# Performance work log

Measured on AMD Instinct MI355X. Metric: run time of the kernel, lower is better.

The kernel has to match this reference:

```python
import jax, jax.numpy as jnp
import numpy as np

B, IN_DIM, D, H, L = 16, 4096, 100, 200, 4
N, E = B * IN_DIM, 8 * B * IN_DIM
EPS = 1e-7  # GENConv message eps


def setup_inputs() -> dict:
    key = jax.random.key(0)
    ks = jax.random.split(key, 16)
    s = 0.05
    return {
        "x": jax.random.normal(ks[0], (N, 1), jnp.float32),
        "edge_index": jax.random.randint(ks[1], (2, E), 0, N),
        "batch_ids": jnp.repeat(jnp.arange(B), IN_DIM),  # graphs of exactly IN_DIM nodes
        "enc_w": jax.random.normal(ks[2], (1, D), jnp.float32) * s,
        "enc_b": jnp.zeros((D,), jnp.float32),
        "h1_w": jax.random.normal(ks[3], (IN_DIM, 1000), jnp.float32) * 0.02,
        "h1_b": jnp.zeros((1000,), jnp.float32),
        "h2_w": jax.random.normal(ks[4], (1000, 100), jnp.float32) * s,
        "h2_b": jnp.zeros((100,), jnp.float32),
        "ln_g": jnp.ones((L, D), jnp.float32),
        "ln_b": jnp.zeros((L, D), jnp.float32),
        "w1": jax.random.normal(ks[5], (L, D, H), jnp.float32) * s,
        "b1": jnp.zeros((L, H), jnp.float32),
        "bn_g": jnp.ones((L, H), jnp.float32),
        "bn_b": jnp.zeros((L, H), jnp.float32),
        "w2": jax.random.normal(ks[6], (L, H, D), jnp.float32) * s,
        "b2": jnp.zeros((L, D), jnp.float32),
        "dec_w": jax.random.normal(ks[7], (D, 1), jnp.float32) * s,
        "dec_b": jnp.zeros((1,), jnp.float32),
    }


def reference(x, edge_index, batch_ids, enc_w, enc_b, h1_w, h1_b, h2_w, h2_b,
              ln_g, ln_b, w1, b1, bn_g, bn_b, w2, b2, dec_w, dec_b):
    src, dst = edge_index[0], edge_index[1]
    # dense branch: [B, IN_DIM] -> 1000 -> 100 with leaky_relu (dropout p=0)
    xs = x.reshape(B, IN_DIM)
    xs = jax.nn.leaky_relu(xs @ h1_w + h1_b, 0.01)
    xs = jax.nn.leaky_relu(xs @ h2_w + h2_b, 0.01)

    h = x @ enc_w + enc_b  # node encoder -> [N, D]
    for i in range(L):  # DeepGCNLayer res+: x + GENConv(dropout(relu(LN(x))))
        mu = jnp.mean(h, axis=-1, keepdims=True)
        var = jnp.mean((h - mu) ** 2, axis=-1, keepdims=True)
        hn = (h - mu) * jax.lax.rsqrt(var + 1e-5) * ln_g[i] + ln_b[i]
        hn = jnp.maximum(hn, 0.0)  # act (dropout in eval mode = identity)
        # GENConv: message = relu(x_j) + eps, softmax aggregation (t=1)
        m = jnp.maximum(hn[src], 0.0) + EPS            # [E, D]
        mx = jax.ops.segment_max(m, dst, num_segments=N)
        ex = jnp.exp(m - mx[dst])
        den = jax.ops.segment_sum(ex, dst, num_segments=N)
        agg = jax.ops.segment_sum((ex / den[dst]) * m, dst, num_segments=N)
        # out = mlp(agg + x): Linear(D,2D) -> BN(eval) -> ReLU -> Linear(2D,D)
        z = (agg + hn) @ w1[i] + b1[i]
        z = jnp.maximum(z * bn_g[i] + bn_b[i], 0.0)
        h = h + (z @ w2[i] + b2[i])

    pooled = jax.ops.segment_sum(h, batch_ids, num_segments=B) / IN_DIM
    out = 0.5 * xs + 0.5 * pooled
    return (out @ dec_w + dec_b)[:, 0]
```

## Files before the change

### kernel.cpp

```cpp
#include <hip/hip_runtime.h>
#include <hip/hip_bf16.h>
#include <hip/hip_fp16.h>
#include <math.h>

#define B_ 16
#define IN_DIM_ 4096
#define D_ 100
#define H_ 200
#define L_ 4
#define N_ (B_*IN_DIM_)
#define E_ (8*B_*IN_DIM_)
#define EPS_ 1e-7f

typedef __attribute__((ext_vector_type(8))) short bf16x8s;
typedef __attribute__((ext_vector_type(4))) float f32x4;

__device__ inline unsigned pack_bf16x2(float a, float b){
  __hip_bfloat16 x = __float2bfloat16(a), y = __float2bfloat16(b);
  unsigned short ux = *(unsigned short*)&x, uy = *(unsigned short*)&y;
  return (unsigned)ux | ((unsigned)uy << 16);
}
__device__ inline __half2 u2h(unsigned v){ return *(__half2*)&v; }

__device__ inline unsigned char f2fp8(float v){
  unsigned p = __builtin_amdgcn_cvt_pk_fp8_f32(v, 0.f, 0u, false);
  return (unsigned char)(p & 0xFF);
}

__global__ void enc_stats_kernel(const float* __restrict__ enc_w,
                                 const float* __restrict__ enc_b,
                                 float* __restrict__ stats) {
  __shared__ float sw[128], sb[128], sww[128], swb[128], sbb[128];
  int t = threadIdx.x;
  float w=0.f, b=0.f;
  if (t < D_){ w = enc_w[t]; b = enc_b[t]; }
  sw[t]=w; sb[t]=b; sww[t]=w*w; swb[t]=w*b; sbb[t]=b*b;
  __syncthreads();
  for (int off=64; off; off>>=1){
    if (t<off){ sw[t]+=sw[t+off]; sb[t]+=sb[t+off]; sww[t]+=sww[t+off];
                swb[t]+=swb[t+off]; sbb[t]+=sbb[t+off]; }
    __syncthreads();
  }
  if (t==0){
    float mw = sw[0]*(1.f/D_), mb = sb[0]*(1.f/D_);
    stats[0]=mw; stats[1]=mb;
    stats[2]=sww[0]*(1.f/D_) - mw*mw;
    stats[3]=swb[0]*(1.f/D_) - mw*mb;
    stats[4]=sbb[0]*(1.f/D_) - mb*mb;
  }
}

#define D1_BLKS_   512
#define ENC_BLKS_  2048
#define DEG_BLKS_  2048
#define PREP_BLKS_ 448
#define SETUP_BLKS_ (D1_BLKS_+ENC_BLKS_+DEG_BLKS_+PREP_BLKS_)

__global__ void setup_kernel(const float* __restrict__ x, const float* __restrict__ enc_w,
                             const float* __restrict__ enc_b, const float* __restrict__ g0,
                             const float* __restrict__ b0, const float* __restrict__ stats,
                             __half* __restrict__ h, char* __restrict__ hnb,
                             char* __restrict__ hnb8,
                             const int* __restrict__ dsts, int* __restrict__ deg,
                             const float* __restrict__ h1_w, float* __restrict__ xs1acc,
                             const float* __restrict__ w1, const float* __restrict__ w2,
                             __hip_bfloat16* __restrict__ w1T, __hip_bfloat16* __restrict__ w2T) {
  __shared__ float xl[16][32];
  int bid = blockIdx.x;
  int t = threadIdx.x;
  if (bid < D1_BLKS_) {
    int bx = bid & 3, by = bid >> 2;
    int k0 = by * 32;
    for (int i = t; i < 16*32; i += 256) {
      int b = i >> 5, kk = i & 31;
      xl[b][kk] = x[b*IN_DIM_ + k0 + kk];
    }
    __syncthreads();
    int c = bx*256 + t;
    if (c >= 1000) return;
    float acc[B_];
    #pragma unroll
    for (int b=0;b<B_;b++) acc[b]=0.f;
    #pragma unroll 4
    for (int kk=0; kk<32; kk++) {
      float w = h1_w[(size_t)(k0+kk)*1000 + c];
      #pragma unroll
      for (int b=0;b<B_;b++) acc[b] += xl[b][kk]*w;
    }
    #pragma unroll
    for (int b=0;b<B_;b++) atomicAdd(&xs1acc[b*1000+c], acc[b]);
  } else if (bid < D1_BLKS_+ENC_BLKS_) {
    int eb = bid - D1_BLKS_;
    int wave = t >> 6, lane = t & 63;
    int base = eb*32 + wave*8;
    float mw = stats[0], mb = stats[1], vw = stats[2], cwb = stats[3], vb = stats[4];
    float xv = 0.f;
    if (lane < 8) xv = x[base + lane];
    int c0 = 2*lane, c1 = c0+1;
    bool v = c0 < D_;
    float ew0=0.f, ew1=0.f, ebv0=0.f, ebv1=0.f, gg0=0.f, gg1=0.f, bv0=0.f, bv1=0.f;
    if (v) { ew0=enc_w[c0]; ew1=enc_w[c1]; ebv0=enc_b[c0]; ebv1=enc_b[c1];
             gg0=g0[c0]; gg1=g0[c1]; bv0=b0[c0]; bv1=b0[c1]; }
    #pragma unroll
    for (int it=0; it<8; ++it) {
      int wid = base + it;
      float xn = __shfl(xv, it, 64);
      float mu = fmaf(xn, mw, mb);
      float var = fmaf(xn*xn, vw, fmaf(2.f*xn, cwb, vb));
      float rstd = rsqrtf(var + 1e-5f);
      float h0 = fmaf(xn, ew0, ebv0);
      float h1 = fmaf(xn, ew1, ebv1);
      if (c0 < 112) *(__half2*)&h[(size_t)wid*112 + c0] = __floats2half2_rn(h0, h1);
      float n0 = v? fmaxf(fmaf((h0-mu)*rstd, gg0, bv0), 0.f) : 0.f;
      float n1 = v? fmaxf(fmaf((h1-mu)*rstd, gg1, bv1), 0.f) : 0.f;
      *(__half2*)(hnb + (size_t)wid*256 + 4*lane) = __floats2half2_rn(n0, n1);
      unsigned short p8 = (unsigned short)f2fp8(n0) | ((unsigned short)f2fp8(n1) << 8);
      *(unsigned short*)(hnb8 + (size_t)wid*128 + c0) = p8;
    }
  } else if (bid < D1_BLKS_+ENC_BLKS_+DEG_BLKS_) {
    int e = (bid - (D1_BLKS_+ENC_BLKS_))*256 + t;
    if (e < E_) atomicAdd(&deg[dsts[e]], 1);
  } else {
    int idx = (bid - (D1_BLKS_+ENC_BLKS_+DEG_BLKS_))*256 + t;
    if (idx < L_*224*128) {
      int l = idx / (224*128);
      int rem = idx % (224*128);
      int col = rem / 128, k = rem % 128;
      float v = (col < H_ && k < D_) ? w1[(l*D_ + k)*H_ + col] : 0.f;
      w1T[idx] = __float2bfloat16(v);
    }
    if (idx < L_*112*224) {
      int l = idx / (112*224);
      int rem = idx % (112*224);
      int col = rem / 224, k = rem % 224;
      float v = (col < D_ && k < H_) ? w2[(l*H_ + k)*D_ + col] : 0.f;
      w2T[idx] = __float2bfloat16(v);
    }
  }
}

__global__ void stage2_kernel(const int* __restrict__ deg, int* __restrict__ row_start,
                              const float* __restrict__ xs1acc, const float* __restrict__ h1_b,
                              const float* __restrict__ h2_w, float* __restrict__ xs2acc,
                              int* __restrict__ hist) {
  __shared__ int sums[1024];
  int t = threadIdx.x;
  int bid = blockIdx.x;
  if (bid == 0) {
    int base = t*64;
    int s = 0;
    for (int j=0;j<64;j++) s += deg[base+j];
    sums[t] = s;
    __syncthreads();
    for (int off=1; off<1024; off<<=1){
      int add = (t>=off)? sums[t-off] : 0;
      __syncthreads();
      sums[t] += add;
      __syncthreads();
    }
    int excl = (t==0)? 0 : sums[t-1];
    int run = excl;
    for (int j=0;j<64;j++){ row_start[base+j] = run; run += deg[base+j]; }
    if (t==1023) row_start[N_] = run;
  } else if (bid <= 4) {
    int T = (bid-1)*1024 + t;
    if (T >= 100*40) return;
    int c = T % 100, kc = T / 100;
    int k0 = kc*25;
    float acc[B_];
    #pragma unroll
    for (int b=0;b<B_;b++) acc[b]=0.f;
    for (int kk=0;kk<25;kk++){
      int k = k0+kk;
      float w = h2_w[k*100 + c];
      float bk = h1_b[k];
      #pragma unroll
      for (int b=0;b<B_;b++){
        float m = xs1acc[b*1000+k] + bk;
        m = (m>0.f)? m : 0.01f*m;
        acc[b] += m*w;
      }
    }
    #pragma unroll
    for (int b=0;b<B_;b++) atomicAdd(&xs2acc[b*100+c], acc[b]);
  } else {
    __shared__ int lh[256];
    if (t < 256) lh[t] = 0;
    __syncthreads();
    int base = (bid-5)*16384;
    for (int n = base + t; n < base + 16384; n += 1024) {
      int d = deg[n]; if (d > 255) d = 255;
      atomicAdd(&lh[d], 1);
    }
    __syncthreads();
    if (t < 256 && lh[t] > 0) atomicAdd(&hist[t], lh[t]);
  }
}

__global__ void binscan_kernel(const int* __restrict__ hist, int* __restrict__ binoff,
                               int* __restrict__ bincnt) {
  __shared__ int s[256];
  int t = threadIdx.x;
  int hv = hist[t];
  s[t] = hv;
  __syncthreads();
  for (int off=1; off<256; off<<=1){
    int v = (t>=off)? s[t-off] : 0;
    __syncthreads();
    s[t] += v;
    __syncthreads();
  }
  binoff[t] = s[t] - hv;
  bincnt[t] = 0;
}

__global__ void scatter_kernel(const int* __restrict__ srcs, const int* __restrict__ dst,
                               const int* __restrict__ row_start, int* __restrict__ cnt,
                               int* __restrict__ sorted_src,
                               const int* __restrict__ deg, const int* __restrict__ binoff,
                               int* __restrict__ bincnt, int* __restrict__ order) {
  int bid = blockIdx.x;
  int t = threadIdx.x;
  if (bid < 2048) {
    int e = bid*256 + t;
    int d = dst[e];
    int p = row_start[d] + atomicAdd(&cnt[d], 1);
    sorted_src[p] = srcs[e];
  } else {
    __shared__ int lh[256], lbase[256];
    int n = (bid-2048)*256 + t;
    int d = deg[n]; int b = (d > 255) ? 255 : d;
    lh[t] = 0;
    __syncthreads();
    int myrank = atomicAdd(&lh[b], 1);
    __syncthreads();
    lbase[t] = (lh[t] > 0) ? atomicAdd(&bincnt[t], lh[t]) : 0;
    __syncthreads();
    order[binoff[b] + lbase[b] + myrank] = n;
  }
}

__global__ void agg_kernel(const char* __restrict__ hnb, const char* __restrict__ hnb8,
                           const int* __restrict__ row_start,
                           const int* __restrict__ sorted_src,
                           const int* __restrict__ order, unsigned* __restrict__ u) {
  int gw = (blockIdx.x*256 + threadIdx.x) >> 6;
  int lane = threadIdx.x & 63;
  int lpos = lane & 31;
  int gbase = lane & 32;
  int node = order[gw*2 + (lane >> 5)];
  int beg = row_start[node];
  int deg = row_start[node+1] - beg;
  int mdeg = deg;
  #pragma unroll
  for (int m=1; m<64; m<<=1) { int o = __shfl_xor(mdeg, m, 64); mdeg = mdeg > o ? mdeg : o; }
  const char* lanep8 = hnb8 + 4*lpos;
  float s0=0.f,s1=0.f,s2=0.f,s3=0.f, w0=0.f,w1=0.f,w2=0.f,w3=0.f;

#define CONSUME_(R) { \
    float v0=__builtin_amdgcn_cvt_f32_fp8(R,0)+EPS_; \
    float v1=__builtin_amdgcn_cvt_f32_fp8(R,1)+EPS_; \
    float v2=__builtin_amdgcn_cvt_f32_fp8(R,2)+EPS_; \
    float v3=__builtin_amdgcn_cvt_f32_fp8(R,3)+EPS_; \
    float e0=__expf(v0), e1=__expf(v1), e2=__expf(v2), e3=__expf(v3); \
    s0+=e0; w0=fmaf(e0,v0,w0); s1+=e1; w1=fmaf(e1,v1,w1); \
    s2+=e2; w2=fmaf(e2,v2,w2); s3+=e3; w3=fmaf(e3,v3,w3); }

  for (int cb=0; cb<mdeg; cb+=32){
    int cidx = (cb + lpos < deg) ? sorted_src[beg + cb + lpos] : 0;
    int cnt = mdeg - cb; if (cnt > 32) cnt = 32;
    int grem = deg - cb;
    int glim = grem < cnt ? grem : cnt; if (glim < 0) glim = 0;
    unsigned r0=0, r1=0, r2=0, r3=0;
    if (0 < glim) r0 = *(const unsigned*)(lanep8 + (size_t)__shfl(cidx, gbase+0)*128);
    if (1 < glim) r1 = *(const unsigned*)(lanep8 + (size_t)__shfl(cidx, gbase+1)*128);
    if (2 < glim) r2 = *(const unsigned*)(lanep8 + (size_t)__shfl(cidx, gbase+2)*128);
    if (3 < glim) r3 = *(const unsigned*)(lanep8 + (size_t)__shfl(cidx, gbase+3)*128);
    for (int j=0; j<cnt; j+=4){
      unsigned n0=0, n1=0, n2=0, n3=0;
      if (j+4 < glim) n0 = *(const unsigned*)(lanep8 + (size_t)__shfl(cidx, gbase+j+4)*128);
      if (j+5 < glim) n1 = *(const unsigned*)(lanep8 + (size_t)__shfl(cidx, gbase+j+5)*128);
      if (j+6 < glim) n2 = *(const unsigned*)(lanep8 + (size_t)__shfl(cidx, gbase+j+6)*128);
      if (j+7 < glim) n3 = *(const unsigned*)(lanep8 + (size_t)__shfl(cidx, gbase+j+7)*128);
      if (j   < glim) CONSUME_(r0);
      if (j+1 < glim) CONSUME_(r1);
      if (j+2 < glim) CONSUME_(r2);
      if (j+3 < glim) CONSUME_(r3);
      r0=n0; r1=n1; r2=n2; r3=n3;
    }
  }
#undef CONSUME_

  uint2 own = *(const uint2*)(hnb + (size_t)node*256 + 8*lpos);
  __half2 oa = u2h(own.x), ob = u2h(own.y);
  float u0 = ((deg>0)? w0/s0 : 0.f) + __low2float(oa);
  float u1 = ((deg>0)? w1/s1 : 0.f) + __high2float(oa);
  float u2 = ((deg>0)? w2/s2 : 0.f) + __low2float(ob);
  float u3 = ((deg>0)? w3/s3 : 0.f) + __high2float(ob);
  if (lpos >= 25) { u0=0.f; u1=0.f; u2=0.f; u3=0.f; }
  uint2 outv; outv.x = pack_bf16x2(u0,u1); outv.y = pack_bf16x2(u2,u3);
  *(uint2*)((char*)u + (size_t)node*256 + 8*lpos) = outv;
}

__global__ __launch_bounds__(256,4) void gemm1_kernel(
    const char* __restrict__ u, const __hip_bfloat16* __restrict__ w1T,
    const float* __restrict__ b1, const float* __restrict__ bng, const float* __restrict__ bnb,
    char* __restrict__ z) {
  __shared__ __align__(16) char wL[112*272];
  int bid = blockIdx.x;
  int half = bid & 1;
  size_t row0 = (size_t)(bid >> 1) * 64;
  int t = threadIdx.x;
  const char* wg = (const char*)w1T + (size_t)half*112*256;
  #pragma unroll
  for (int c = t; c < 1792; c += 256) {
    int r = c >> 4, sb = (c & 15) << 4;
    *(float4*)(wL + r*272 + sb) = *(const float4*)(wg + (size_t)r*256 + sb);
  }
  __syncthreads();
  int wave = t >> 6, lane = t & 63;
  int l15 = lane & 15;
  int kgb = (lane >> 4) << 4;
  int ar = wave*16 + l15;
  bf16x8s a[4];
  #pragma unroll
  for (int ks=0; ks<4; ks++)
    a[ks] = *(const bf16x8s*)(u + (row0 + ar)*256 + ks*64 + kgb);
  f32x4 acc[7];
  #pragma unroll
  for (int n=0;n<7;n++) acc[n] = (f32x4){0.f,0.f,0.f,0.f};
  #pragma unroll
  for (int ks=0; ks<4; ks++) {
    int kb = ks*64 + kgb;
    #pragma unroll
    for (int n=0;n<7;n++) {
      bf16x8s b = *(const bf16x8s*)(wL + (n*16 + l15)*272 + kb);
      acc[n] = __builtin_amdgcn_mfma_f32_16x16x32_bf16(a[ks], b, acc[n], 0, 0, 0);
    }
  }
  size_t rbase = row0 + wave*16 + ((lane>>4)<<2);
  #pragma unroll
  for (int n=0;n<7;n++) {
    int col = half*112 + n*16 + l15;
    float bias = (col < H_) ? b1[col] : 0.f;
    float g    = (col < H_) ? bng[col] : 0.f;
    float bb   = (col < H_) ? bnb[col] : 0.f;
    #pragma unroll
    for (int r=0;r<4;r++) {
      float v = fmaxf((acc[n][r] + bias)*g + bb, 0.f);
      if (col >= H_) v = 0.f;
      *(__hip_bfloat16*)(z + (rbase + r)*448 + 2*col) = __float2bfloat16(v);
    }
  }
}

template<int LAST>
__global__ __launch_bounds__(256,3) void gemm2_kernel(
    const char* __restrict__ z, const __hip_bfloat16* __restrict__ w2T,
    const float* __restrict__ b2, __half* __restrict__ h,
    const float* __restrict__ lng, const float* __restrict__ lnb,
    char* __restrict__ hnb, char* __restrict__ hnb8, float* __restrict__ pooled) {
  __shared__ __align__(16) char wL[112*464];
  int t = threadIdx.x;
  size_t row0 = (size_t)blockIdx.x * 64;
  const char* wg = (const char*)w2T;
  for (int c = t; c < 3136; c += 256) {
    int r = c / 28, sb = (c - r*28) << 4;
    *(float4*)(wL + r*464 + sb) = *(const float4*)(wg + (size_t)r*448 + sb);
  }
  __syncthreads();
  int wave = t >> 6, lane = t & 63;
  int l15 = lane & 15;
  int kgb = (lane >> 4) << 4;
  int ar = wave*16 + l15;
  bf16x8s a[7];
  #pragma unroll
  for (int ks=0; ks<7; ks++)
    a[ks] = *(const bf16x8s*)(z + (row0 + ar)*448 + ks*64 + kgb);
  f32x4 acc[7];
  #pragma unroll
  for (int n=0;n<7;n++) acc[n] = (f32x4){0.f,0.f,0.f,0.f};
  #pragma unroll
  for (int ks=0; ks<7; ks++) {
    int kb = ks*64 + kgb;
    #pragma unroll
    for (int n=0;n<7;n++) {
      bf16x8s b = *(const bf16x8s*)(wL + (n*16 + l15)*464 + kb);
      acc[n] = __builtin_amdgcn_mfma_f32_16x16x32_bf16(a[ks], b, acc[n], 0, 0, 0);
    }
  }
  size_t rbase = row0 + wave*16 + ((lane>>4)<<2);

  float x_[7][4];
  float sum[4]  = {0,0,0,0};
  float sum2[4] = {0,0,0,0};
  float psum[7] = {0,0,0,0,0,0,0};
  #pragma unroll
  for (int n=0;n<7;n++) {
    int col = n*16 + l15;
    bool valid = col < D_;
    float bias = valid ? b2[col] : 0.f;
    #pragma unroll
    for (int r=0;r<4;r++) {
      float xv = 0.f;
      if (valid) xv = acc[n][r] + bias + __half2float(h[(rbase + r)*112 + col]);
      x_[n][r] = xv;
      if (LAST) {
        psum[n] += xv;
      } else {
        sum[r] += xv; sum2[r] += xv*xv;
        if (valid) h[(rbase + r)*112 + col] = __float2half(xv);
      }
    }
  }

  if (LAST) {
    #pragma unroll
    for (int n=0;n<7;n++) {
      psum[n] += __shfl_xor(psum[n], 16, 64);
      psum[n] += __shfl_xor(psum[n], 32, 64);
    }
    __syncthreads();
    float* ps = (float*)wL;
    if (lane < 16) {
      #pragma unroll
      for (int n=0;n<7;n++) ps[wave*112 + n*16 + l15] = psum[n];
    }
    __syncthreads();
    if (t < D_) {
      float v = ps[t] + ps[112+t] + ps[224+t] + ps[336+t];
      int b = (int)(row0 >> 12);
      atomicAdd(&pooled[b*D_ + t], v);
    }
  } else {
    #pragma unroll
    for (int r=0;r<4;r++) {
      float s = sum[r], s2 = sum2[r];
      #pragma unroll
      for (int m=1;m<16;m<<=1) { s += __shfl_xor(s, m, 16); s2 += __shfl_xor(s2, m, 16); }
      sum[r] = s; sum2[r] = s2;
    }
    #pragma unroll
    for (int n=0;n<7;n++) {
      int col = n*16 + l15;
      float g  = (col < D_) ? lng[col] : 0.f;
      float be = (col < D_) ? lnb[col] : 0.f;
      #pragma unroll
      for (int r=0;r<4;r++) {
        float mu = sum[r]*(1.f/D_);
        float var = sum2[r]*(1.f/D_) - mu*mu;
        float rstd = rsqrtf(var + 1e-5f);
        float hv = fmaxf(fmaf((x_[n][r]-mu)*rstd, g, be), 0.f);
        if (col >= D_) hv = 0.f;
        *(__half*)(hnb + (rbase + r)*256 + 2*col) = __float2half(hv);
        *(unsigned char*)(hnb8 + (rbase + r)*128 + col) = f2fp8(hv);
      }
    }
    {
      int col = 112 + l15;
      __half zh = __float2half(0.f);
      #pragma unroll
      for (int r=0;r<4;r++) {
        *(__half*)(hnb + (rbase + r)*256 + 2*col) = zh;
        *(unsigned char*)(hnb8 + (rbase + r)*128 + col) = 0;
      }
    }
  }
}

__global__ void final_kernel(const float* __restrict__ xs2acc, const float* __restrict__ h2_b,
                             const float* __restrict__ pooled,
                             const float* __restrict__ dec_w, const float* __restrict__ dec_b,
                             float* __restrict__ out) {
  __shared__ float red[128];
  int t = threadIdx.x;
  for (int b=0;b<B_;b++){
    float v = 0.f;
    if (t < D_) {
      float xs = xs2acc[b*D_+t] + h2_b[t];
      xs = (xs>0.f)? xs : 0.01f*xs;
      v = (0.5f*xs + (0.5f/IN_DIM_)*pooled[b*D_+t]) * dec_w[t];
    }
    red[t] = v;
    __syncthreads();
    for (int off=64; off; off>>=1){
      if (t < off) red[t] += red[t+off];
      __syncthreads();
    }
    if (t==0) out[b] = red[0] + dec_b[0];
    __syncthreads();
  }
}

extern "C" void kernel_launch(void* const* d_in, const int* in_sizes, int n_in,
                              void* d_out, int out_size, void* d_ws, size_t ws_size,
                              hipStream_t stream) {
  const float* x      = (const float*)d_in[0];
  const int*   eidx   = (const int*)d_in[1];
  const float* enc_w  = (const float*)d_in[3];
  const float* enc_b  = (const float*)d_in[4];
  const float* h1_w   = (const float*)d_in[5];
  const float* h1_b   = (const float*)d_in[6];
  const float* h2_w   = (const float*)d_in[7];
  const float* h2_b   = (const float*)d_in[8];
  const float* ln_g   = (const float*)d_in[9];
  const float* ln_b   = (const float*)d_in[10];
  const float* w1     = (const float*)d_in[11];
  const float* b1     = (const float*)d_in[12];
  const float* bn_g   = (const float*)d_in[13];
  const float* bn_b   = (const float*)d_in[14];
  const float* w2     = (const float*)d_in[15];
  const float* b2     = (const float*)d_in[16];
  const float* dec_w  = (const float*)d_in[17];
  const float* dec_b  = (const float*)d_in[18];
  float* out = (float*)d_out;

  char* ws = (char*)d_ws;
  size_t off = 0;
  auto alloc = [&](size_t bytes)->char* {
    char* p = ws + off;
    off += (bytes + 255) & ~(size_t)255;
    return p;
  };
  __half* h     = (__half*)alloc((size_t)N_*112*2);
  char*  hnb    = alloc((size_t)N_*256);
  char*  hnb8   = alloc((size_t)N_*128);
  char*  z      = alloc((size_t)N_*448);
  unsigned* u   = (unsigned*)alloc((size_t)N_*64*4);
  __hip_bfloat16* w1T = (__hip_bfloat16*)alloc((size_t)L_*224*128*2);
  __hip_bfloat16* w2T = (__hip_bfloat16*)alloc((size_t)L_*112*224*2);
  size_t zbsz = 64000 + 6400 + 6400 + (size_t)N_*4 + (size_t)N_*4 + 1024;
  char* zb = alloc(zbsz);
  float* xs1    = (float*)zb;
  float* xs2    = (float*)(zb + 64000);
  float* pooled = (float*)(zb + 64000 + 6400);
  int* deg      = (int*)(zb + 64000 + 6400 + 6400);
  int* cnt      = (int*)(zb + 64000 + 6400 + 6400 + (size_t)N_*4);
  int* hist     = (int*)(zb + 64000 + 6400 + 6400 + (size_t)N_*8);
  int* row_start  = (int*)alloc((N_+1)*4);
  int* sorted_src = (int*)alloc((size_t)E_*4);
  int* order      = (int*)alloc((size_t)N_*4);
  int* binoff     = (int*)alloc(1024);
  int* bincnt     = (int*)alloc(1024);
  float* stats    = (float*)alloc(256);

  const int* srcs = eidx;
  const int* dsts = eidx + E_;

  hipMemsetAsync(zb, 0, zbsz, stream);

  enc_stats_kernel<<<1, 128, 0, stream>>>(enc_w, enc_b, stats);
  setup_kernel<<<SETUP_BLKS_, 256, 0, stream>>>(x, enc_w, enc_b, ln_g, ln_b, stats,
                                                h, hnb, hnb8,
                                                dsts, deg, h1_w, xs1, w1, w2, w1T, w2T);
  stage2_kernel<<<9, 1024, 0, stream>>>(deg, row_start, xs1, h1_b, h2_w, xs2, hist);
  binscan_kernel<<<1, 256, 0, stream>>>(hist, binoff, bincnt);
  scatter_kernel<<<2048+256, 256, 0, stream>>>(srcs, dsts, row_start, cnt, sorted_src,
                                               deg, binoff, bincnt, order);

  for (int i=0;i<L_;i++){
    agg_kernel<<<N_/8, 256, 0, stream>>>(hnb, hnb8, row_start, sorted_src, order, u);
    gemm1_kernel<<<(N_/64)*2, 256, 0, stream>>>((const char*)u,
                                                w1T + (size_t)i*224*128, b1 + i*H_,
                                                bn_g + i*H_, bn_b + i*H_, z);
    if (i < L_-1) {
      gemm2_kernel<0><<<N_/64, 256, 0, stream>>>(z, w2T + (size_t)i*112*224, b2 + i*D_,
                                                 h, ln_g + (i+1)*D_, ln_b + (i+1)*D_,
                                                 hnb, hnb8, pooled);
    } else {
      gemm2_kernel<1><<<N_/64, 256, 0, stream>>>(z, w2T + (size_t)i*112*224, b2 + i*D_,
                                                 h, nullptr, nullptr, hnb, hnb8, pooled);
    }
  }

  final_kernel<<<1, 128, 0, stream>>>(xs2, h2_b, pooled, dec_w, dec_b, out);
}
```

Baseline: 398.2 us.

## Store gemm1 output in fp8, fuse final reduction into last gemm2, simplify degree max

The hidden activation z between the two MLP GEMMs is stored as fp8 instead of bf16, halving its write and read traffic; gemm2 converts it back to bf16 for MFMA. The final decoder kernel is merged into the last gemm2 using a completion counter so the last block computes outputs. The aggregation kernel's max-degree reduction is reduced to one cross-half shuffle. Fp8 storage of z reduces precision of the intermediate activations.

```diff
diff --git a/kernel.cpp b/kernel.cpp
--- a/kernel.cpp
+++ b/kernel.cpp
@@ -251,9 +251,8 @@
   int node = order[gw*2 + (lane >> 5)];
   int beg = row_start[node];
   int deg = row_start[node+1] - beg;
-  int mdeg = deg;
-  #pragma unroll
-  for (int m=1; m<64; m<<=1) { int o = __shfl_xor(mdeg, m, 64); mdeg = mdeg > o ? mdeg : o; }
+  int dother = __shfl_xor(deg, 32, 64);
+  int mdeg = deg > dother ? deg : dother;
   const char* lanep8 = hnb8 + 4*lpos;
   float s0=0.f,s1=0.f,s2=0.f,s3=0.f, w0=0.f,w1=0.f,w2=0.f,w3=0.f;
 
@@ -305,7 +304,7 @@
 __global__ __launch_bounds__(256,4) void gemm1_kernel(
     const char* __restrict__ u, const __hip_bfloat16* __restrict__ w1T,
     const float* __restrict__ b1, const float* __restrict__ bng, const float* __restrict__ bnb,
-    char* __restrict__ z) {
+    char* __restrict__ z8) {
   __shared__ __align__(16) char wL[112*272];
   int bid = blockIdx.x;
   int half = bid & 1;
@@ -349,17 +348,21 @@
     for (int r=0;r<4;r++) {
       float v = fmaxf((acc[n][r] + bias)*g + bb, 0.f);
       if (col >= H_) v = 0.f;
-      *(__hip_bfloat16*)(z + (rbase + r)*448 + 2*col) = __float2bfloat16(v);
+      *(unsigned char*)(z8 + (rbase + r)*224 + col) = f2fp8(v);
     }
   }
 }
 
 template<int LAST>
 __global__ __launch_bounds__(256,3) void gemm2_kernel(
-    const char* __restrict__ z, const __hip_bfloat16* __restrict__ w2T,
+    const char* __restrict__ z8, const __hip_bfloat16* __restrict__ w2T,
     const float* __restrict__ b2, __half* __restrict__ h,
     const float* __restrict__ lng, const float* __restrict__ lnb,
-    char* __restrict__ hnb, char* __restrict__ hnb8, float* __restrict__ pooled) {
+    char* __restrict__ hnb, char* __restrict__ hnb8, float* __restrict__ pooled,
+    int* __restrict__ done,
+    const float* __restrict__ xs2acc, const float* __restrict__ h2_b,
+    const float* __restrict__ dec_w, const float* __restrict__ dec_b,
+    float* __restrict__ out) {
   __shared__ __align__(16) char wL[112*464];
   int t = threadIdx.x;
   size_t row0 = (size_t)blockIdx.x * 64;
@@ -374,9 +377,22 @@
   int kgb = (lane >> 4) << 4;
   int ar = wave*16 + l15;
   bf16x8s a[7];
-  #pragma unroll
-  for (int ks=0; ks<7; ks++)
-    a[ks] = *(const bf16x8s*)(z + (row0 + ar)*448 + ks*64 + kgb);
+  {
+    const char* zrow = z8 + (row0 + ar)*224;
+    int g8 = (lane >> 4) << 3;
+    #pragma unroll
+    for (int ks=0; ks<7; ks++) {
+      uint2 p = *(const uint2*)(zrow + ks*32 + g8);
+      float f0=__builtin_amdgcn_cvt_f32_fp8(p.x,0), f1=__builtin_amdgcn_cvt_f32_fp8(p.x,1);
+      float f2=__builtin_amdgcn_cvt_f32_fp8(p.x,2), f3=__builtin_amdgcn_cvt_f32_fp8(p.x,3);
+      float f4=__builtin_amdgcn_cvt_f32_fp8(p.y,0), f5=__builtin_amdgcn_cvt_f32_fp8(p.y,1);
+      float f6=__builtin_amdgcn_cvt_f32_fp8(p.y,2), f7=__builtin_amdgcn_cvt_f32_fp8(p.y,3);
+      uint4 q;
+      q.x = pack_bf16x2(f0,f1); q.y = pack_bf16x2(f2,f3);
+      q.z = pack_bf16x2(f4,f5); q.w = pack_bf16x2(f6,f7);
+      a[ks] = *(bf16x8s*)&q;
+    }
+  }
   f32x4 acc[7];
   #pragma unroll
   for (int n=0;n<7;n++) acc[n] = (f32x4){0.f,0.f,0.f,0.f};
@@ -431,6 +447,31 @@
       float v = ps[t] + ps[112+t] + ps[224+t] + ps[336+t];
       int b = (int)(row0 >> 12);
       atomicAdd(&pooled[b*D_ + t], v);
+    }
+    __threadfence();
+    __shared__ int lastflag;
+    if (t == 0) lastflag = (atomicAdd(done, 1) == gridDim.x - 1) ? 1 : 0;
+    __syncthreads();
+    if (lastflag) {
+      __threadfence();
+      float* red = (float*)wL;
+      for (int b=0;b<B_;b++){
+        float v = 0.f;
+        if (t < D_) {
+          float pv = atomicAdd(&pooled[b*D_+t], 0.f);
+          float xs = xs2acc[b*D_+t] + h2_b[t];
+          xs = (xs>0.f)? xs : 0.01f*xs;
+          v = (0.5f*xs + (0.5f/IN_DIM_)*pv) * dec_w[t];
+        }
+        if (t < 128) red[t] = v;
+        __syncthreads();
+        for (int off=64; off; off>>=1){
+          if (t < off) red[t] += red[t+off];
+          __syncthreads();
+        }
+        if (t==0) out[b] = red[0] + dec_b[0];
+        __syncthreads();
+      }
     }
   } else {
     #pragma unroll
@@ -465,30 +506,6 @@
         *(unsigned char*)(hnb8 + (rbase + r)*128 + col) = 0;
       }
     }
-  }
-}
-
-__global__ void final_kernel(const float* __restrict__ xs2acc, const float* __restrict__ h2_b,
-                             const float* __restrict__ pooled,
-                             const float* __restrict__ dec_w, const float* __restrict__ dec_b,
-                             float* __restrict__ out) {
-  __shared__ float red[128];
-  int t = threadIdx.x;
-  for (int b=0;b<B_;b++){
-    float v = 0.f;
-    if (t < D_) {
-      float xs = xs2acc[b*D_+t] + h2_b[t];
-      xs = (xs>0.f)? xs : 0.01f*xs;
-      v = (0.5f*xs + (0.5f/IN_DIM_)*pooled[b*D_+t]) * dec_w[t];
-    }
-    red[t] = v;
-    __syncthreads();
-    for (int off=64; off; off>>=1){
-      if (t < off) red[t] += red[t+off];
-      __syncthreads();
-    }
-    if (t==0) out[b] = red[0] + dec_b[0];
-    __syncthreads();
   }
 }
 
@@ -525,11 +542,11 @@
   __half* h     = (__half*)alloc((size_t)N_*112*2);
   char*  hnb    = alloc((size_t)N_*256);
   char*  hnb8   = alloc((size_t)N_*128);
-  char*  z      = alloc((size_t)N_*448);
+  char*  z8     = alloc((size_t)N_*224);
   unsigned* u   = (unsigned*)alloc((size_t)N_*64*4);
   __hip_bfloat16* w1T = (__hip_bfloat16*)alloc((size_t)L_*224*128*2);
   __hip_bfloat16* w2T = (__hip_bfloat16*)alloc((size_t)L_*112*224*2);
-  size_t zbsz = 64000 + 6400 + 6400 + (size_t)N_*4 + (size_t)N_*4 + 1024;
+  size_t zbsz = 64000 + 6400 + 6400 + (size_t)N_*4 + (size_t)N_*4 + 1024 + 256;
   char* zb = alloc(zbsz);
   float* xs1    = (float*)zb;
   float* xs2    = (float*)(zb + 64000);
@@ -537,6 +554,7 @@
   int* deg      = (int*)(zb + 64000 + 6400 + 6400);
   int* cnt      = (int*)(zb + 64000 + 6400 + 6400 + (size_t)N_*4);
   int* hist     = (int*)(zb + 64000 + 6400 + 6400 + (size_t)N_*8);
+  int* done     = (int*)(zb + 64000 + 6400 + 6400 + (size_t)N_*8 + 1024);
   int* row_start  = (int*)alloc((N_+1)*4);
   int* sorted_src = (int*)alloc((size_t)E_*4);
   int* order      = (int*)alloc((size_t)N_*4);
@@ -562,16 +580,16 @@
     agg_kernel<<<N_/8, 256, 0, stream>>>(hnb, hnb8, row_start, sorted_src, order, u);
     gemm1_kernel<<<(N_/64)*2, 256, 0, stream>>>((const char*)u,
                                                 w1T + (size_t)i*224*128, b1 + i*H_,
-                                                bn_g + i*H_, bn_b + i*H_, z);
+                                                bn_g + i*H_, bn_b + i*H_, z8);
     if (i < L_-1) {
-      gemm2_kernel<0><<<N_/64, 256, 0, stream>>>(z, w2T + (size_t)i*112*224, b2 + i*D_,
+      gemm2_kernel<0><<<N_/64, 256, 0, stream>>>(z8, w2T + (size_t)i*112*224, b2 + i*D_,
                                                  h, ln_g + (i+1)*D_, ln_b + (i+1)*D_,
-                                                 hnb, hnb8, pooled);
+                                                 hnb, hnb8, pooled, done,
+                                                 nullptr, nullptr, nullptr, nullptr, nullptr);
     } else {
-      gemm2_kernel<1><<<N_/64, 256, 0, stream>>>(z, w2T + (size_t)i*112*224, b2 + i*D_,
-                                                 h, nullptr, nullptr, hnb, hnb8, pooled);
-    }
-  }
-
-  final_kernel<<<1, 128, 0, stream>>>(xs2, h2_b, pooled, dec_w, dec_b, out);
-}
+      gemm2_kernel<1><<<N_/64, 256, 0, stream>>>(z8, w2T + (size_t)i*112*224, b2 + i*D_,
+                                                 h, nullptr, nullptr, hnb, hnb8, pooled, done,
+                                                 xs2, h2_b, dec_w, dec_b, out);
+    }
+  }
+}
```

Result: slower. 454.2 us (+14.1%).
